# Optimization experiments

Measured on AMD Instinct MI355X. Metric: run time of the kernel, lower is better.

Reference implementation:

```python
import jax, jax.numpy as jnp
import numpy as np

B, S, D, H = 2, 2048, 1024, 16
DH = D // H  # 64


def setup_inputs() -> dict:
    key = jax.random.key(0)
    k1, k2, k3, k4 = jax.random.split(key, 4)
    x = jax.random.normal(k1, (B, S, D), dtype=jnp.float32)
    # causal mask: 0 => masked (matches mask==0 -> -inf in source)
    mask = jnp.tril(jnp.ones((S, S), dtype=jnp.int32))
    Wq = jax.random.normal(k2, (H, D, DH), dtype=jnp.float32) * (D ** -0.5)
    Wk = jax.random.normal(k3, (H, D, DH), dtype=jnp.float32) * (D ** -0.5)
    Wo = jax.random.normal(k4, (D, D), dtype=jnp.float32) * (D ** -0.5)
    bo = jnp.zeros((D,), dtype=jnp.float32)
    return {"x": x, "mask": mask, "Wq": Wq, "Wk": Wk, "Wo": Wo, "bo": bo}


def reference(x, mask, Wq, Wk, Wo, bo):
    # Per source: q = query(x), k = key(x), v = query(x)  (bug kept: v == q)
    q = jnp.einsum('bsd,hde->bhse', x, Wq)   # [B,H,S,DH]
    k = jnp.einsum('bsd,hde->bhse', x, Wk)   # [B,H,S,DH]
    # scale uses d_model (input dim), not d_head -- faithful to source
    scale = jnp.asarray(D, x.dtype) ** -0.5
    scores = jnp.einsum('bhse,bhte->bhst', q, k) * scale  # [B,H,S,S]
    neg_inf = jnp.asarray(float('-inf'), scores.dtype)
    scores = jnp.where(mask[None, None, :, :] == 0, neg_inf, scores)
    w = jax.nn.softmax(scores, axis=-1)
    attn = jnp.einsum('bhst,bhte->bhse', w, q)  # v == q
    # concat heads: head axis becomes contiguous feature blocks
    attn = attn.transpose(0, 2, 1, 3).reshape(B, S, D)
    return attn @ Wo + bo
```

## Files before the change

kernel.cpp:

```cpp
#include <hip/hip_runtime.h>
#include <hip/hip_bf16.h>

#define BQ 2
#define SQ 2048
#define DMODEL 1024
#define NH 16
#define DH 64
#define NQT (SQ / 64)

typedef __attribute__((ext_vector_type(8))) short bf16x8;
typedef __attribute__((ext_vector_type(4))) short bf16x4;
typedef __attribute__((ext_vector_type(4))) float f32x4;
typedef unsigned short u16;

__device__ __forceinline__ u16 f2b(float f) {
  __hip_bfloat16 h = __float2bfloat16(f);
  return *reinterpret_cast<u16*>(&h);
}

__device__ __forceinline__ unsigned packbf(float lo, float hi) {
  return ((unsigned)f2b(hi) << 16) | (unsigned)f2b(lo);
}

#define MFMA(a, b, c) __builtin_amdgcn_mfma_f32_16x16x32_bf16((a), (b), (c), 0, 0, 0)

__device__ __forceinline__ f32x4 mfma16(bf16x4 a, bf16x4 b, f32x4 c) {
  asm("v_mfma_f32_16x16x16_bf16 %0, %1, %2, %0" : "+v"(c) : "v"(a), "v"(b));
  return c;
}

__device__ __forceinline__ unsigned cvtpk(float lo, float hi) {
  unsigned r;
  asm("v_cvt_pk_bf16_f32 %0, %1, %2" : "=v"(r) : "v"(lo), "v"(hi));
  return r;
}

#define CS (0.03125f * 1.44269504088896f)


__global__ void cvt_x_kernel(const float* __restrict__ x, u16* __restrict__ xb, int n) {
  int i = blockIdx.x * blockDim.x + threadIdx.x;
  int stride = gridDim.x * blockDim.x;
  for (; i < n; i += stride) xb[i] = f2b(x[i]);
}

__global__ __launch_bounds__(256) void prep_w_kernel(
    const float* __restrict__ Wq, const float* __restrict__ Wk,
    const float* __restrict__ Wo,
    u16* __restrict__ WqT, u16* __restrict__ WkT, u16* __restrict__ WoT) {
  __shared__ alignas(16) u16 T[64][72];
  int xt = blockIdx.x, yt = blockIdx.y, z = blockIdx.z;
  int tid = threadIdx.x;
  if (z < 2) {
    const float* W = z ? Wk : Wq;
    u16* WT = z ? WkT : WqT;
    const float* src = W + ((size_t)yt * 1024 + xt * 64) * 64;
#pragma unroll
    for (int i = 0; i < 4; ++i) {
      int lin = tid + i * 256;
      int r = lin >> 4, c4 = (lin & 15) * 4;
      float4 v = *(const float4*)&src[(size_t)r * 64 + c4];
      *(unsigned*)&T[r][c4]     = packbf(v.x, v.y);
      *(unsigned*)&T[r][c4 + 2] = packbf(v.z, v.w);
    }
    __syncthreads();
#pragma unroll
    for (int i = 0; i < 2; ++i) {
      int lin = tid + i * 256;
      int e = lin >> 3, d8 = (lin & 7) * 8;
      u16 tmp[8];
#pragma unroll
      for (int j = 0; j < 8; ++j) tmp[j] = T[d8 + j][e];
      *(uint4*)&WT[((size_t)yt * 64 + e) * 1024 + xt * 64 + d8] = *(uint4*)tmp;
    }
  } else {
    const float* src = Wo + ((size_t)xt * 64) * 1024 + yt * 64;
#pragma unroll
    for (int i = 0; i < 4; ++i) {
      int lin = tid + i * 256;
      int r = lin >> 4, c4 = (lin & 15) * 4;
      float4 v = *(const float4*)&src[(size_t)r * 1024 + c4];
      *(unsigned*)&T[r][c4]     = packbf(v.x, v.y);
      *(unsigned*)&T[r][c4 + 2] = packbf(v.z, v.w);
    }
    __syncthreads();
#pragma unroll
    for (int i = 0; i < 2; ++i) {
      int lin = tid + i * 256;
      int n = lin >> 3, k8 = (lin & 7) * 8;
      u16 tmp[8];
#pragma unroll
      for (int j = 0; j < 8; ++j) tmp[j] = T[k8 + j][n];
      *(uint4*)&WoT[((size_t)yt * 64 + n) * 1024 + xt * 64 + k8] = *(uint4*)tmp;
    }
  }
}

__global__ __launch_bounds__(256) void transpose_q_kernel(
    const u16* __restrict__ Q, u16* __restrict__ QT) {
  __shared__ alignas(16) u16 T[64][72];
  int st = blockIdx.x, h = blockIdx.y, b = blockIdx.z;
  size_t hb = ((size_t)(b * NH + h)) * SQ * DH;
  int tid = threadIdx.x;
#pragma unroll
  for (int i2 = 0; i2 < 2; ++i2) {
    int c = tid + i2 * 256;
    int r = c >> 3, cc = (c & 7) * 8;
    *(uint4*)&T[r][cc] = *(const uint4*)&Q[hb + (size_t)(st * 64 + r) * DH + cc];
  }
  __syncthreads();
#pragma unroll
  for (int i2 = 0; i2 < 2; ++i2) {
    int c = tid + i2 * 256;
    int e = c >> 3, s8 = (c & 7) * 8;
    u16 tmp[8];
#pragma unroll
    for (int j = 0; j < 8; ++j) tmp[j] = T[s8 + j][e];
    *(uint4*)&QT[hb + (size_t)e * SQ + st * 64 + s8] = *(uint4*)tmp;
  }
}


__global__ __launch_bounds__(256) void proj_kernel(
    const u16* __restrict__ xb,
    const u16* __restrict__ Wcat,
    u16* __restrict__ Qb, u16* __restrict__ Kb,
    u16* __restrict__ QT) {
  __shared__ alignas(16) u16 Xs[64][72];
  __shared__ alignas(16) u16 Ws[64][72];
  int st = blockIdx.x, hy = blockIdx.y, b = blockIdx.z;
  int tid = threadIdx.x, w = tid >> 6, l = tid & 63;
  int lr = l & 15, hi = l >> 4, lk = hi * 8;
  int r0s = tid >> 3, cc0 = (tid & 7) * 8, r1s = r0s + 32;
  f32x4 acc[4] = {};
  const u16* Ab = xb + (size_t)(b * SQ + st * 64) * DMODEL;
  const u16* Wb = Wcat + (size_t)hy * DH * DMODEL;

  *(uint4*)&Xs[r0s][cc0] = *(const uint4*)&Ab[(size_t)r0s * DMODEL + cc0];
  *(uint4*)&Xs[r1s][cc0] = *(const uint4*)&Ab[(size_t)r1s * DMODEL + cc0];
  *(uint4*)&Ws[r0s][cc0] = *(const uint4*)&Wb[(size_t)r0s * DMODEL + cc0];
  *(uint4*)&Ws[r1s][cc0] = *(const uint4*)&Wb[(size_t)r1s * DMODEL + cc0];
  __syncthreads();

  uint4 xr0 = *(const uint4*)&Ab[(size_t)r0s * DMODEL + 64 + cc0];
  uint4 xr1 = *(const uint4*)&Ab[(size_t)r1s * DMODEL + 64 + cc0];
  uint4 wv0 = *(const uint4*)&Wb[(size_t)r0s * DMODEL + 64 + cc0];
  uint4 wv1 = *(const uint4*)&Wb[(size_t)r1s * DMODEL + 64 + cc0];

  for (int ks = 0; ks < 16; ++ks) {
#pragma unroll
    for (int kk = 0; kk < 2; ++kk) {
      bf16x8 a = *(const bf16x8*)&Xs[w * 16 + lr][kk * 32 + lk];
#pragma unroll
      for (int n = 0; n < 4; ++n) {
        bf16x8 bb = *(const bf16x8*)&Ws[n * 16 + lr][kk * 32 + lk];
        acc[n] = MFMA(a, bb, acc[n]);
      }
    }
    if (ks < 15) {
      __syncthreads();
      *(uint4*)&Xs[r0s][cc0] = xr0;
      *(uint4*)&Xs[r1s][cc0] = xr1;
      *(uint4*)&Ws[r0s][cc0] = wv0;
      *(uint4*)&Ws[r1s][cc0] = wv1;
      if (ks + 2 < 16) {
        int k0 = (ks + 2) * 64;
        xr0 = *(const uint4*)&Ab[(size_t)r0s * DMODEL + k0 + cc0];
        xr1 = *(const uint4*)&Ab[(size_t)r1s * DMODEL + k0 + cc0];
        wv0 = *(const uint4*)&Wb[(size_t)r0s * DMODEL + k0 + cc0];
        wv1 = *(const uint4*)&Wb[(size_t)r1s * DMODEL + k0 + cc0];
      }
      __syncthreads();
    }
  }

  bool isQ = (hy < NH);
  float scale = isQ ? 1.0f : CS;
  int hh = hy & (NH - 1);
  size_t hbh = ((size_t)(b * NH + hh)) * SQ * DH;
  size_t obase = hbh + (size_t)st * 64 * DH;
  int r0 = w * 16 + (hi << 2);
  u16 (*Cs)[72] = Xs;
  __syncthreads();
#pragma unroll
  for (int n = 0; n < 4; ++n)
#pragma unroll
    for (int r = 0; r < 4; ++r)
      Cs[r0 + r][n * 16 + lr] = f2b(acc[n][r] * scale);
  __syncthreads();

  u16* dst = isQ ? Qb : Kb;
#pragma unroll
  for (int i2 = 0; i2 < 2; ++i2) {
    int lin = tid + i2 * 256;
    int r = lin >> 3, c8 = (lin & 7) * 8;
    *(uint4*)&dst[obase + (size_t)r * DH + c8] = *(const uint4*)&Cs[r][c8];
  }
  if (isQ && QT) {
#pragma unroll
    for (int i2 = 0; i2 < 2; ++i2) {
      int lin = tid + i2 * 256;
      int e = lin >> 3, s8 = (lin & 7) * 8;
      u16 tmp[8];
#pragma unroll
      for (int j = 0; j < 8; ++j) tmp[j] = Cs[s8 + j][e];
      *(uint4*)&QT[hbh + (size_t)e * SQ + st * 64 + s8] = *(uint4*)tmp;
    }
  }
}


__global__ __launch_bounds__(512) void attn_kernel(
    const u16* __restrict__ Qt,
    const u16* __restrict__ Kt,
    const u16* __restrict__ QTt,
    u16* __restrict__ Oc) {
  __shared__ alignas(16) u16 Ks[2][64][72];
  __shared__ alignas(16) u16 Vs[2][64][72];
  int bx = blockIdx.x, h = blockIdx.y, b = blockIdx.z;
  int p = b ? bx : (15 - bx);
  int tid = threadIdx.x, w = tid >> 6, l = tid & 63;
  int lr = l & 15, hi = l >> 4, lk = hi * 8;
  int qtile = 2 * p + (w >> 2);
  int q0 = qtile * 64 + (w & 3) * 16;
  int jmax = 2 * p + 1;
  size_t hb = ((size_t)(b * NH + h)) * SQ * DH;

  int r0s = tid >> 3, cc0 = (tid & 7) * 8;

  bf16x8 aq[2];
  {
    const u16* qrow = Qt + hb + (size_t)(q0 + lr) * DH;
    aq[0] = *(const bf16x8*)&qrow[lk];
    aq[1] = *(const bf16x8*)&qrow[32 + lk];
  }

  *(uint4*)&Ks[0][r0s][cc0] = *(const uint4*)&Kt[hb + (size_t)r0s * DH + cc0];
  *(uint4*)&Vs[0][r0s][cc0] = *(const uint4*)&QTt[hb + (size_t)r0s * SQ + cc0];
  __syncthreads();

  uint4 kreg = *(const uint4*)&Kt[hb + (size_t)(64 + r0s) * DH + cc0];
  uint4 vreg = *(const uint4*)&QTt[hb + (size_t)r0s * SQ + 64 + cc0];

  f32x4 acc_t[4] = {};
  float l_run = 0.f;
  int cur = 0;

  for (int j = 0; j <= jmax; ++j) {
    if (j <= qtile) {
      f32x4 s[4] = {};
#pragma unroll
      for (int kk = 0; kk < 2; ++kk)
#pragma unroll
        for (int n = 0; n < 4; ++n) {
          bf16x8 bk = *(const bf16x8*)&Ks[cur][n * 16 + lr][kk * 32 + lk];
          s[n] = MFMA(bk, aq[kk], s[n]);
        }

      if (j == qtile) {
        int qg = q0 + lr;
#pragma unroll
        for (int n = 0; n < 4; ++n) {
          int kbase = j * 64 + n * 16 + hi * 4;
#pragma unroll
          for (int r = 0; r < 4; ++r)
            s[n][r] = (kbase + r > qg) ? 0.f : exp2f(s[n][r]);
        }
      } else {
#pragma unroll
        for (int n = 0; n < 4; ++n)
#pragma unroll
          for (int r = 0; r < 4; ++r) s[n][r] = exp2f(s[n][r]);
      }

#pragma unroll
      for (int n = 0; n < 4; ++n)
        l_run += (s[n][0] + s[n][1]) + (s[n][2] + s[n][3]);

      bf16x4 pb[4];
#pragma unroll
      for (int n = 0; n < 4; ++n) {
        uint2 u;
        u.x = cvtpk(s[n][0], s[n][1]);
        u.y = cvtpk(s[n][2], s[n][3]);
        pb[n] = *(bf16x4*)&u;
      }

#pragma unroll
      for (int nv = 0; nv < 4; ++nv) {
        const u16* vrow = &Vs[cur][nv * 16 + lr][hi * 4];
#pragma unroll
        for (int nh = 0; nh < 4; ++nh) {
          bf16x4 va = *(const bf16x4*)&vrow[nh * 16];
          acc_t[nv] = mfma16(va, pb[nh], acc_t[nv]);
        }
      }
    }

    if (j < jmax) {
      *(uint4*)&Ks[cur ^ 1][r0s][cc0] = kreg;
      *(uint4*)&Vs[cur ^ 1][r0s][cc0] = vreg;
      if (j + 2 <= jmax) {
        kreg = *(const uint4*)&Kt[hb + (size_t)((j + 2) * 64 + r0s) * DH + cc0];
        vreg = *(const uint4*)&QTt[hb + (size_t)r0s * SQ + (j + 2) * 64 + cc0];
      }
      __syncthreads();
      cur ^= 1;
    }
  }

  l_run += __shfl_xor(l_run, 16, 64);
  l_run += __shfl_xor(l_run, 32, 64);
  float inv = 1.f / l_run;

  size_t rbase = ((size_t)b * SQ + q0 + lr) * DMODEL + h * DH;
#pragma unroll
  for (int nv = 0; nv < 4; ++nv) {
#pragma unroll
    for (int rp = 0; rp < 2; ++rp) {
      unsigned pw = cvtpk(acc_t[nv][2 * rp] * inv, acc_t[nv][2 * rp + 1] * inv);
      *(unsigned*)&Oc[rbase + nv * 16 + hi * 4 + 2 * rp] = pw;
    }
  }
}


__global__ __launch_bounds__(256) void outproj_kernel(
    const u16* __restrict__ Oc,
    const u16* __restrict__ WoT,
    const float* __restrict__ bo,
    float* __restrict__ out) {
  __shared__ alignas(16) u16 Xs[64][72];
  __shared__ alignas(16) u16 Ws[64][72];
  int rt = blockIdx.x, nt = blockIdx.y;
  int tid = threadIdx.x, w = tid >> 6, l = tid & 63;
  int lr = l & 15, lk = (l >> 4) * 8;
  int r0s = tid >> 3, cc0 = (tid & 7) * 8, r1s = r0s + 32;
  f32x4 acc[4] = {};
  const u16* Ab = Oc + (size_t)rt * 64 * DMODEL;
  const u16* Wb = WoT + (size_t)nt * 64 * DMODEL;

  *(uint4*)&Xs[r0s][cc0] = *(const uint4*)&Ab[(size_t)r0s * DMODEL + cc0];
  *(uint4*)&Xs[r1s][cc0] = *(const uint4*)&Ab[(size_t)r1s * DMODEL + cc0];
  *(uint4*)&Ws[r0s][cc0] = *(const uint4*)&Wb[(size_t)r0s * DMODEL + cc0];
  *(uint4*)&Ws[r1s][cc0] = *(const uint4*)&Wb[(size_t)r1s * DMODEL + cc0];
  __syncthreads();

  uint4 xr0 = *(const uint4*)&Ab[(size_t)r0s * DMODEL + 64 + cc0];
  uint4 xr1 = *(const uint4*)&Ab[(size_t)r1s * DMODEL + 64 + cc0];
  uint4 wv0 = *(const uint4*)&Wb[(size_t)r0s * DMODEL + 64 + cc0];
  uint4 wv1 = *(const uint4*)&Wb[(size_t)r1s * DMODEL + 64 + cc0];

  for (int ks = 0; ks < 16; ++ks) {
#pragma unroll
    for (int kk = 0; kk < 2; ++kk) {
      bf16x8 a = *(const bf16x8*)&Xs[w * 16 + lr][kk * 32 + lk];
#pragma unroll
      for (int n = 0; n < 4; ++n) {
        bf16x8 bb = *(const bf16x8*)&Ws[n * 16 + lr][kk * 32 + lk];
        acc[n] = MFMA(a, bb, acc[n]);
      }
    }
    if (ks < 15) {
      __syncthreads();
      *(uint4*)&Xs[r0s][cc0] = xr0;
      *(uint4*)&Xs[r1s][cc0] = xr1;
      *(uint4*)&Ws[r0s][cc0] = wv0;
      *(uint4*)&Ws[r1s][cc0] = wv1;
      if (ks + 2 < 16) {
        int k0 = (ks + 2) * 64;
        xr0 = *(const uint4*)&Ab[(size_t)r0s * DMODEL + k0 + cc0];
        xr1 = *(const uint4*)&Ab[(size_t)r1s * DMODEL + k0 + cc0];
        wv0 = *(const uint4*)&Wb[(size_t)r0s * DMODEL + k0 + cc0];
        wv1 = *(const uint4*)&Wb[(size_t)r1s * DMODEL + k0 + cc0];
      }
      __syncthreads();
    }
  }

  int r0 = w * 16 + ((l >> 4) << 2);
#pragma unroll
  for (int n = 0; n < 4; ++n) {
    int col = nt * 64 + n * 16 + lr;
    float bv = bo[col];
#pragma unroll
    for (int r = 0; r < 4; ++r)
      out[(size_t)(rt * 64 + r0 + r) * DMODEL + col] = acc[n][r] + bv;
  }
}


extern "C" void kernel_launch(void* const* d_in, const int* in_sizes, int n_in,
                              void* d_out, int out_size, void* d_ws, size_t ws_size,
                              hipStream_t stream) {
  const float* x  = (const float*)d_in[0];
  const float* Wq = (const float*)d_in[2];
  const float* Wk = (const float*)d_in[3];
  const float* Wo = (const float*)d_in[4];
  const float* bo = (const float*)d_in[5];
  float* out = (float*)d_out;

  char* ws = (char*)d_ws;
  u16* xb  = (u16*)ws;
  u16* WqT = xb + (size_t)BQ * SQ * DMODEL;
  u16* WkT = WqT + (size_t)NH * DH * DMODEL;
  u16* WoT = WkT + (size_t)NH * DH * DMODEL;
  u16* Qb  = WoT + (size_t)DMODEL * DMODEL;
  u16* Kb  = Qb + (size_t)BQ * NH * SQ * DH;
  u16* Ob  = Kb + (size_t)BQ * NH * SQ * DH;
  u16* QTnew = Ob + (size_t)BQ * SQ * DMODEL;

  size_t need = ((size_t)QTnew - (size_t)ws) + (size_t)BQ * SQ * DMODEL * sizeof(u16);
  bool fused = ws_size >= need;
  u16* QTb = fused ? QTnew : xb;

  cvt_x_kernel<<<2048, 256, 0, stream>>>(x, xb, BQ * SQ * DMODEL);
  prep_w_kernel<<<dim3(16, 16, 3), 256, 0, stream>>>(Wq, Wk, Wo, WqT, WkT, WoT);

  proj_kernel<<<dim3(SQ / 64, 2 * NH, BQ), 256, 0, stream>>>(
      xb, WqT, Qb, Kb, fused ? QTb : (u16*)nullptr);
  if (!fused)
    transpose_q_kernel<<<dim3(SQ / 64, NH, BQ), 256, 0, stream>>>(Qb, QTb);
  attn_kernel<<<dim3(16, NH, BQ), 512, 0, stream>>>(Qb, Kb, QTb, Ob);
  outproj_kernel<<<dim3(BQ * SQ / 64, DMODEL / 64, 1), 256, 0, stream>>>(Ob, WoT, bo, out);
}
```

Baseline: 110.5 us.

## Software-pipeline QK^T of the next tile with softmax and PV of the previous

Restructures the attention loop so each iteration issues the QK^T MFMAs for tile j while running exp, row-sum and the PV MFMAs on the scores kept from tile j-1. The loop gets one extra drain iteration. V shared-memory buffers go from two to three so the previous tile's V stays valid while the next one is written. The goal is to overlap matrix-core work with transcendental and VALU work inside each wave, at the cost of more live registers and extra LDS.

```diff
diff --git a/kernel.cpp b/kernel.cpp
--- a/kernel.cpp
+++ b/kernel.cpp
@@ -216,7 +216,7 @@
     const u16* __restrict__ QTt,
     u16* __restrict__ Oc) {
   __shared__ alignas(16) u16 Ks[2][64][72];
-  __shared__ alignas(16) u16 Vs[2][64][72];
+  __shared__ alignas(16) u16 Vs[3][64][72];
   int bx = blockIdx.x, h = blockIdx.y, b = blockIdx.z;
   int p = b ? bx : (15 - bx);
   int tid = threadIdx.x, w = tid >> 6, l = tid & 63;
@@ -243,52 +243,57 @@
   uint4 vreg = *(const uint4*)&QTt[hb + (size_t)r0s * SQ + 64 + cc0];
 
   f32x4 acc_t[4] = {};
+  f32x4 s_prev[4] = {};
   float l_run = 0.f;
   int cur = 0;
 
-  for (int j = 0; j <= jmax; ++j) {
-    if (j <= qtile) {
-      f32x4 s[4] = {};
+  for (int j = 0; j <= jmax + 1; ++j) {
+    f32x4 s_new[4] = {};
+    if (j <= jmax && j <= qtile) {
 #pragma unroll
       for (int kk = 0; kk < 2; ++kk)
 #pragma unroll
         for (int n = 0; n < 4; ++n) {
           bf16x8 bk = *(const bf16x8*)&Ks[cur][n * 16 + lr][kk * 32 + lk];
-          s[n] = MFMA(bk, aq[kk], s[n]);
+          s_new[n] = MFMA(bk, aq[kk], s_new[n]);
         }
-
-      if (j == qtile) {
+    }
+
+    int t = j - 1;
+    if (t >= 0 && t <= qtile) {
+      if (t == qtile) {
         int qg = q0 + lr;
 #pragma unroll
         for (int n = 0; n < 4; ++n) {
-          int kbase = j * 64 + n * 16 + hi * 4;
+          int kbase = t * 64 + n * 16 + hi * 4;
 #pragma unroll
           for (int r = 0; r < 4; ++r)
-            s[n][r] = (kbase + r > qg) ? 0.f : exp2f(s[n][r]);
+            s_prev[n][r] = (kbase + r > qg) ? 0.f : exp2f(s_prev[n][r]);
         }
       } else {
 #pragma unroll
         for (int n = 0; n < 4; ++n)
 #pragma unroll
-          for (int r = 0; r < 4; ++r) s[n][r] = exp2f(s[n][r]);
+          for (int r = 0; r < 4; ++r) s_prev[n][r] = exp2f(s_prev[n][r]);
       }
 
 #pragma unroll
       for (int n = 0; n < 4; ++n)
-        l_run += (s[n][0] + s[n][1]) + (s[n][2] + s[n][3]);
+        l_run += (s_prev[n][0] + s_prev[n][1]) + (s_prev[n][2] + s_prev[n][3]);
 
       bf16x4 pb[4];
 #pragma unroll
       for (int n = 0; n < 4; ++n) {
         uint2 u;
-        u.x = cvtpk(s[n][0], s[n][1]);
-        u.y = cvtpk(s[n][2], s[n][3]);
+        u.x = cvtpk(s_prev[n][0], s_prev[n][1]);
+        u.y = cvtpk(s_prev[n][2], s_prev[n][3]);
         pb[n] = *(bf16x4*)&u;
       }
 
+      const u16* vbuf = &Vs[t % 3][0][0];
 #pragma unroll
       for (int nv = 0; nv < 4; ++nv) {
-        const u16* vrow = &Vs[cur][nv * 16 + lr][hi * 4];
+        const u16* vrow = vbuf + (size_t)(nv * 16 + lr) * 72 + hi * 4;
 #pragma unroll
         for (int nh = 0; nh < 4; ++nh) {
           bf16x4 va = *(const bf16x4*)&vrow[nh * 16];
@@ -297,9 +302,12 @@
       }
     }
 
+#pragma unroll
+    for (int n = 0; n < 4; ++n) s_prev[n] = s_new[n];
+
     if (j < jmax) {
       *(uint4*)&Ks[cur ^ 1][r0s][cc0] = kreg;
-      *(uint4*)&Vs[cur ^ 1][r0s][cc0] = vreg;
+      *(uint4*)&Vs[(j + 1) % 3][r0s][cc0] = vreg;
       if (j + 2 <= jmax) {
         kreg = *(const uint4*)&Kt[hb + (size_t)((j + 2) * 64 + r0s) * DH + cc0];
         vreg = *(const uint4*)&QTt[hb + (size_t)r0s * SQ + (j + 2) * 64 + cc0];
```

Result: slower. 116.3 us (+5.2%).

## Split attention blocks to one query tile per 256-thread block

Applied to the files above, without the earlier changes.

The attention kernel changes from 512-thread blocks that each cover a pair of query tiles to 256-thread blocks that each cover one 64-row query tile. The grid grows from 16 to 32 blocks along the tile axis, and tiles are launched from the longest to the shortest causal extent. Each thread now stages two rows of K and V per tile, and the per-warp qtile guard inside the loop goes away. This should raise block count and occupancy and drop the wasted loop iterations of the shorter tile in each pair. The cost is that K/V tiles are loaded once per query tile instead of being shared by two tiles.

```diff
diff --git a/kernel.cpp b/kernel.cpp
--- a/kernel.cpp
+++ b/kernel.cpp
@@ -210,7 +210,7 @@
 }
 
 
-__global__ __launch_bounds__(512) void attn_kernel(
+__global__ __launch_bounds__(256) void attn_kernel(
     const u16* __restrict__ Qt,
     const u16* __restrict__ Kt,
     const u16* __restrict__ QTt,
@@ -218,15 +218,15 @@
   __shared__ alignas(16) u16 Ks[2][64][72];
   __shared__ alignas(16) u16 Vs[2][64][72];
   int bx = blockIdx.x, h = blockIdx.y, b = blockIdx.z;
-  int p = b ? bx : (15 - bx);
   int tid = threadIdx.x, w = tid >> 6, l = tid & 63;
   int lr = l & 15, hi = l >> 4, lk = hi * 8;
-  int qtile = 2 * p + (w >> 2);
-  int q0 = qtile * 64 + (w & 3) * 16;
-  int jmax = 2 * p + 1;
+  int qtile = NQT - 1 - bx;
+  int q0 = qtile * 64 + w * 16;
+  int jmax = qtile;
   size_t hb = ((size_t)(b * NH + h)) * SQ * DH;
 
   int r0s = tid >> 3, cc0 = (tid & 7) * 8;
+  int r1s = r0s + 32;
 
   bf16x8 aq[2];
   {
@@ -236,73 +236,82 @@
   }
 
   *(uint4*)&Ks[0][r0s][cc0] = *(const uint4*)&Kt[hb + (size_t)r0s * DH + cc0];
+  *(uint4*)&Ks[0][r1s][cc0] = *(const uint4*)&Kt[hb + (size_t)r1s * DH + cc0];
   *(uint4*)&Vs[0][r0s][cc0] = *(const uint4*)&QTt[hb + (size_t)r0s * SQ + cc0];
-  __syncthreads();
-
-  uint4 kreg = *(const uint4*)&Kt[hb + (size_t)(64 + r0s) * DH + cc0];
-  uint4 vreg = *(const uint4*)&QTt[hb + (size_t)r0s * SQ + 64 + cc0];
+  *(uint4*)&Vs[0][r1s][cc0] = *(const uint4*)&QTt[hb + (size_t)r1s * SQ + cc0];
+  __syncthreads();
+
+  uint4 kp0, kp1, vp0, vp1;
+  if (jmax >= 1) {
+    kp0 = *(const uint4*)&Kt[hb + (size_t)(64 + r0s) * DH + cc0];
+    kp1 = *(const uint4*)&Kt[hb + (size_t)(64 + r1s) * DH + cc0];
+    vp0 = *(const uint4*)&QTt[hb + (size_t)r0s * SQ + 64 + cc0];
+    vp1 = *(const uint4*)&QTt[hb + (size_t)r1s * SQ + 64 + cc0];
+  }
 
   f32x4 acc_t[4] = {};
   float l_run = 0.f;
   int cur = 0;
 
   for (int j = 0; j <= jmax; ++j) {
-    if (j <= qtile) {
-      f32x4 s[4] = {};
-#pragma unroll
-      for (int kk = 0; kk < 2; ++kk)
-#pragma unroll
-        for (int n = 0; n < 4; ++n) {
-          bf16x8 bk = *(const bf16x8*)&Ks[cur][n * 16 + lr][kk * 32 + lk];
-          s[n] = MFMA(bk, aq[kk], s[n]);
-        }
-
-      if (j == qtile) {
-        int qg = q0 + lr;
-#pragma unroll
-        for (int n = 0; n < 4; ++n) {
-          int kbase = j * 64 + n * 16 + hi * 4;
-#pragma unroll
-          for (int r = 0; r < 4; ++r)
-            s[n][r] = (kbase + r > qg) ? 0.f : exp2f(s[n][r]);
-        }
-      } else {
-#pragma unroll
-        for (int n = 0; n < 4; ++n)
-#pragma unroll
-          for (int r = 0; r < 4; ++r) s[n][r] = exp2f(s[n][r]);
-      }
-
+    f32x4 s[4] = {};
+#pragma unroll
+    for (int kk = 0; kk < 2; ++kk)
+#pragma unroll
+      for (int n = 0; n < 4; ++n) {
+        bf16x8 bk = *(const bf16x8*)&Ks[cur][n * 16 + lr][kk * 32 + lk];
+        s[n] = MFMA(bk, aq[kk], s[n]);
+      }
+
+    if (j == qtile) {
+      int qg = q0 + lr;
+#pragma unroll
+      for (int n = 0; n < 4; ++n) {
+        int kbase = j * 64 + n * 16 + hi * 4;
+#pragma unroll
+        for (int r = 0; r < 4; ++r)
+          s[n][r] = (kbase + r > qg) ? 0.f : exp2f(s[n][r]);
+      }
+    } else {
 #pragma unroll
       for (int n = 0; n < 4; ++n)
-        l_run += (s[n][0] + s[n][1]) + (s[n][2] + s[n][3]);
-
-      bf16x4 pb[4];
-#pragma unroll
-      for (int n = 0; n < 4; ++n) {
-        uint2 u;
-        u.x = cvtpk(s[n][0], s[n][1]);
-        u.y = cvtpk(s[n][2], s[n][3]);
-        pb[n] = *(bf16x4*)&u;
-      }
-
-#pragma unroll
-      for (int nv = 0; nv < 4; ++nv) {
-        const u16* vrow = &Vs[cur][nv * 16 + lr][hi * 4];
-#pragma unroll
-        for (int nh = 0; nh < 4; ++nh) {
-          bf16x4 va = *(const bf16x4*)&vrow[nh * 16];
-          acc_t[nv] = mfma16(va, pb[nh], acc_t[nv]);
-        }
+#pragma unroll
+        for (int r = 0; r < 4; ++r) s[n][r] = exp2f(s[n][r]);
+    }
+
+#pragma unroll
+    for (int n = 0; n < 4; ++n)
+      l_run += (s[n][0] + s[n][1]) + (s[n][2] + s[n][3]);
+
+    bf16x4 pb[4];
+#pragma unroll
+    for (int n = 0; n < 4; ++n) {
+      uint2 u;
+      u.x = cvtpk(s[n][0], s[n][1]);
+      u.y = cvtpk(s[n][2], s[n][3]);
+      pb[n] = *(bf16x4*)&u;
+    }
+
+#pragma unroll
+    for (int nv = 0; nv < 4; ++nv) {
+      const u16* vrow = &Vs[cur][nv * 16 + lr][hi * 4];
+#pragma unroll
+      for (int nh = 0; nh < 4; ++nh) {
+        bf16x4 va = *(const bf16x4*)&vrow[nh * 16];
+        acc_t[nv] = mfma16(va, pb[nh], acc_t[nv]);
       }
     }
 
     if (j < jmax) {
-      *(uint4*)&Ks[cur ^ 1][r0s][cc0] = kreg;
-      *(uint4*)&Vs[cur ^ 1][r0s][cc0] = vreg;
+      *(uint4*)&Ks[cur ^ 1][r0s][cc0] = kp0;
+      *(uint4*)&Ks[cur ^ 1][r1s][cc0] = kp1;
+      *(uint4*)&Vs[cur ^ 1][r0s][cc0] = vp0;
+      *(uint4*)&Vs[cur ^ 1][r1s][cc0] = vp1;
       if (j + 2 <= jmax) {
-        kreg = *(const uint4*)&Kt[hb + (size_t)((j + 2) * 64 + r0s) * DH + cc0];
-        vreg = *(const uint4*)&QTt[hb + (size_t)r0s * SQ + (j + 2) * 64 + cc0];
+        kp0 = *(const uint4*)&Kt[hb + (size_t)((j + 2) * 64 + r0s) * DH + cc0];
+        kp1 = *(const uint4*)&Kt[hb + (size_t)((j + 2) * 64 + r1s) * DH + cc0];
+        vp0 = *(const uint4*)&QTt[hb + (size_t)r0s * SQ + (j + 2) * 64 + cc0];
+        vp1 = *(const uint4*)&QTt[hb + (size_t)r1s * SQ + (j + 2) * 64 + cc0];
       }
       __syncthreads();
       cur ^= 1;
@@ -421,6 +430,6 @@
       xb, WqT, Qb, Kb, fused ? QTb : (u16*)nullptr);
   if (!fused)
     transpose_q_kernel<<<dim3(SQ / 64, NH, BQ), 256, 0, stream>>>(Qb, QTb);
-  attn_kernel<<<dim3(16, NH, BQ), 512, 0, stream>>>(Qb, Kb, QTb, Ob);
+  attn_kernel<<<dim3(NQT, NH, BQ), 256, 0, stream>>>(Qb, Kb, QTb, Ob);
   outproj_kernel<<<dim3(BQ * SQ / 64, DMODEL / 64, 1), 256, 0, stream>>>(Ob, WoT, bo, out);
 }
```

Result: slower. 134.1 us (+21.4%).
